# Kernel tuning notes

Hardware: AMD Instinct MI355X
Metric: run time of the kernel (lower is better)

Reference implementation:

```python
import math
import jax, jax.numpy as jnp
import numpy as np

NTYPE, C, H, E = 3, 256, 8, 32  # n_embd=256, n_head=8, edge_dim=32
A1 = 16  # aux_x1 feature dim (aux_x2 dim = E - A1)


def setup_inputs() -> dict:
    key = jax.random.key(0)
    ks = jax.random.split(key, 16)
    B, T1, T2 = 8, 128, 256
    s = 0.02
    return {
        "x1": jax.random.normal(ks[0], (B, T1, C), jnp.float32),
        "x2": jax.random.normal(ks[1], (B, T2, C), jnp.float32),
        "aux_x1": jax.random.normal(ks[2], (B, T1, A1), jnp.float32),
        "aux_x2": jax.random.normal(ks[3], (B, T2, E - A1), jnp.float32),
        "masks": jax.random.randint(ks[4], (NTYPE, B, T1, T2), 0, 2, jnp.int32),
        # per-type linear params, stored (in, out) so y = x @ W + b
        "Wq": jax.random.normal(ks[5], (NTYPE, C, C), jnp.float32) * s,
        "bq": jnp.zeros((NTYPE, C), jnp.float32),
        "Wk": jax.random.normal(ks[6], (NTYPE, C + E, C), jnp.float32) * s,
        "bk": jnp.zeros((NTYPE, C), jnp.float32),
        "Wv": jax.random.normal(ks[7], (NTYPE, C + E, C), jnp.float32) * s,
        "bv": jnp.zeros((NTYPE, C), jnp.float32),
        "Wp": jax.random.normal(ks[8], (NTYPE, C, C), jnp.float32) * s,
        "bp": jnp.zeros((NTYPE, C), jnp.float32),
    }


def _aux_attn(x1, x2, aux_x1, aux_x2, mask, Wq, bq, Wk, bk, Wv, bv, Wp, bp):
    """One AuxCrossAttention type. mask: (B,T1,T2) int."""
    B, T1, _ = x1.shape
    T2 = x2.shape[1]
    hd = C // H
    scale = 1.0 / math.sqrt(hd)

    q = x1 @ Wq + bq  # (B,T1,C)
    # k/v over aug_x2 = [x2 | aux_x1 | aux_x2]; split the linear instead of
    # materializing the (B,T1,T2,C+E) concat (same math by linearity).
    Wk_x, Wk_a1, Wk_a2 = Wk[:C], Wk[C:C + A1], Wk[C + A1:]
    Wv_x, Wv_a1, Wv_a2 = Wv[:C], Wv[C:C + A1], Wv[C + A1:]
    k = (x2 @ Wk_x + aux_x2 @ Wk_a2 + bk)[:, None] + (aux_x1 @ Wk_a1)[:, :, None]  # (B,T1,T2,C)
    v = (x2 @ Wv_x + aux_x2 @ Wv_a2 + bv)[:, None] + (aux_x1 @ Wv_a1)[:, :, None]  # (B,T1,T2,C)

    qh = q.reshape(B, T1, H, hd)
    kh = k.reshape(B, T1, T2, H, hd)
    vh = v.reshape(B, T1, T2, H, hd)

    att = jnp.einsum("bthd,btshd->bhts", qh, kh) * scale  # (B,H,T1,T2)
    valid = (mask != 0)[:, None]  # (B,1,T1,T2)
    att = jnp.where(valid, att, -jnp.inf)
    all_masked = (mask == 0).all(-1)  # (B,T1)
    att = jnp.where(all_masked[:, None, :, None], 0.0, att)
    f = jnp.finfo(att.dtype)
    att = jnp.nan_to_num(att, nan=0.0, posinf=f.max, neginf=f.min)
    att = jax.nn.softmax(att, axis=-1)

    y = jnp.einsum("bhts,btshd->bthd", att, vh).reshape(B, T1, C)
    return y @ Wp + bp


def reference(x1, x2, aux_x1, aux_x2, masks, Wq, bq, Wk, bk, Wv, bv, Wp, bp):
    resid = jnp.zeros_like(x1)
    for i in range(NTYPE):
        resid = resid + _aux_attn(x1, x2, aux_x1, aux_x2, masks[i],
                                  Wq[i], bq[i], Wk[i], bk[i], Wv[i], bv[i], Wp[i], bp[i])
    return resid
```

## Files before the change

kernel.cpp:

```cpp
#include <hip/hip_runtime.h>
#include <hip/hip_bf16.h>

#define NC 256
#define HD 32

typedef __attribute__((ext_vector_type(8))) short short8;
typedef __attribute__((ext_vector_type(4))) short short4v;
typedef __attribute__((ext_vector_type(4))) float f32x4;

__device__ __forceinline__ unsigned short f2bf(float f) {
    union { float f; unsigned u; } v; v.f = f;
    unsigned r = v.u + 0x7fffu + ((v.u >> 16) & 1u);
    return (unsigned short)(r >> 16);
}
__device__ __forceinline__ short8 cvt8(float4 a, float4 b) {
    short8 s;
    s[0] = (short)f2bf(a.x); s[1] = (short)f2bf(a.y);
    s[2] = (short)f2bf(a.z); s[3] = (short)f2bf(a.w);
    s[4] = (short)f2bf(b.x); s[5] = (short)f2bf(b.y);
    s[6] = (short)f2bf(b.z); s[7] = (short)f2bf(b.w);
    return s;
}

__global__ __launch_bounds__(256) void prep_a(
    const float* __restrict__ x1, const float* __restrict__ x2,
    const float* __restrict__ ax1, const float* __restrict__ ax2,
    const int* __restrict__ masks,
    short* __restrict__ x1b, short* __restrict__ A2, short* __restrict__ ax1p,
    unsigned int* __restrict__ mb)
{
    const int bx = blockIdx.x, tid = threadIdx.x;
    const short8 zero8 = {0, 0, 0, 0, 0, 0, 0, 0};

    if (bx < 64) {
        const size_t base = ((size_t)bx * 256 + tid) * 16;
        const float* p = x1 + base;
        float4 a = *(const float4*)p,       b = *(const float4*)(p + 4);
        float4 c = *(const float4*)(p + 8), d = *(const float4*)(p + 12);
        *(short8*)&x1b[base]     = cvt8(a, b);
        *(short8*)&x1b[base + 8] = cvt8(c, d);
    } else if (bx < 352) {
        const int g = (bx - 64) * 256 + tid;
        const int row = g / 36, c8 = g - row * 36;
        short8 s;
        if (c8 < 32) {
            const float* p = x2 + (size_t)row * 256 + c8 * 8;
            s = cvt8(*(const float4*)p, *(const float4*)(p + 4));
        } else if (c8 < 34) {
            const float* p = ax2 + (size_t)row * 16 + (c8 - 32) * 8;
            s = cvt8(*(const float4*)p, *(const float4*)(p + 4));
        } else {
            s = zero8;
        }
        *(short8*)&A2[(size_t)row * 288 + c8 * 8] = s;
    } else if (bx < 356) {
        const int row = (bx - 352) * 256 + tid;
        const float* p = ax1 + (size_t)row * 16;
        float4 a = *(const float4*)p,       b = *(const float4*)(p + 4);
        float4 c = *(const float4*)(p + 8), d = *(const float4*)(p + 12);
        short* o = ax1p + (size_t)row * 32;
        *(short8*)o        = cvt8(a, b);
        *(short8*)(o + 8)  = cvt8(c, d);
        *(short8*)(o + 16) = zero8;
        *(short8*)(o + 24) = zero8;
    } else {
        const int r0 = (bx - 356) * 16;
        const int wave = tid >> 6, lane = tid & 63;
        for (int rr = 0; rr < 16; ++rr) {
            const int row = r0 + rr;
            const int mk = masks[(size_t)row * 256 + tid];
            unsigned long long bal = __ballot(mk != 0);
            if (lane == 0) {
                mb[row * 8 + wave * 2 + 0] = (unsigned int)bal;
                mb[row * 8 + wave * 2 + 1] = (unsigned int)(bal >> 32);
            }
        }
    }
}

__global__ __launch_bounds__(256) void prep_w(
    const float* __restrict__ Wq, const float* __restrict__ Wk,
    const float* __restrict__ Wv, const float* __restrict__ Wp,
    short* __restrict__ WqT, short* __restrict__ WkT, short* __restrict__ WvT,
    short* __restrict__ WvA1T, short* __restrict__ WpT)
{
    const int bx = blockIdx.x, n = threadIdx.x;

    if (bx < 96) {
        const int i = bx >> 5, k8 = bx & 31;
        const float* W = Wq + (size_t)i * 256 * 256;
        short8 s;
#pragma unroll
        for (int j = 0; j < 8; ++j) s[j] = (short)f2bf(W[(size_t)(k8 * 8 + j) * 256 + n]);
        *(short8*)&WqT[(size_t)i * 256 * 256 + (size_t)n * 256 + k8 * 8] = s;
    } else if (bx < 312) {
        const int idx0 = bx - 96;
        const int kv = idx0 / 108, idx = idx0 % 108;
        const int i = idx / 36, k8 = idx % 36;
        const float* W = (kv ? Wv : Wk) + (size_t)i * 288 * 256;
        short* O = (kv ? WvT : WkT) + (size_t)i * 256 * 288;
        short8 s;
#pragma unroll
        for (int j = 0; j < 8; ++j) {
            const int kp = k8 * 8 + j;
            const int src = (kp < 256) ? kp : (kp < 272 ? kp + 16 : -1);
            s[j] = (src >= 0) ? (short)f2bf(W[(size_t)src * 256 + n]) : (short)0;
        }
        *(short8*)&O[(size_t)n * 288 + k8 * 8] = s;
    } else if (bx < 408) {
        const int idx = bx - 312, i = idx >> 5, k8 = idx & 31;
        const float* W = Wp + (size_t)i * 256 * 256;
        short8 s;
#pragma unroll
        for (int j = 0; j < 8; ++j) s[j] = (short)f2bf(W[(size_t)(k8 * 8 + j) * 256 + n]);
        *(short8*)&WpT[(size_t)i * 256 * 256 + (size_t)n * 256 + k8 * 8] = s;
    } else {
        const int i = bx - 408;
        const float* W = Wv + (size_t)i * 288 * 256;
        short* O = WvA1T + (size_t)i * 256 * 32 + (size_t)n * 32;
#pragma unroll
        for (int k8 = 0; k8 < 4; ++k8) {
            short8 s;
#pragma unroll
            for (int j = 0; j < 8; ++j) {
                const int kp = k8 * 8 + j;
                s[j] = (kp < 16) ? (short)f2bf(W[(size_t)(256 + kp) * 256 + n]) : (short)0;
            }
            *(short8*)&O[k8 * 8] = s;
        }
    }
}

__global__ __launch_bounds__(256) void fused_gemm(
    const short* __restrict__ x1b, const short* __restrict__ A2,
    const short* __restrict__ ax1p,
    const short* __restrict__ WqT, const short* __restrict__ WkT,
    const short* __restrict__ WvT, const short* __restrict__ WvA1T,
    const float* __restrict__ bq, const float* __restrict__ bk,
    const float* __restrict__ bv,
    short* __restrict__ qb, short* __restrict__ kbb,
    short* __restrict__ vbT, float* __restrict__ va)
{
    const int bx = blockIdx.x;
    const short *Ab, *Wb;
    const float* bias = nullptr;
    short* outb = nullptr; float* outf = nullptr;
    int LDA, LDW, nsteps, mode, m0, n0;
    if (bx < 48) {
        const int i = bx >> 4, t = bx & 15;
        m0 = (t >> 1) * 128; n0 = (t & 1) * 128;
        Ab = x1b; LDA = 256; Wb = WqT + (size_t)i * 256 * 256; LDW = 256;
        nsteps = 8; bias = bq + i * 256; outb = qb + (size_t)i * 1024 * 256; mode = 0;
    } else if (bx < 144) {
        const int idx = bx - 48, i = idx >> 5, t = idx & 31;
        m0 = (t >> 1) * 128; n0 = (t & 1) * 128;
        Ab = A2; LDA = 288; Wb = WkT + (size_t)i * 256 * 288; LDW = 288;
        nsteps = 9; bias = bk + i * 256; outb = kbb + (size_t)i * 2048 * 256; mode = 0;
    } else if (bx < 240) {
        const int idx = bx - 144, i = idx >> 5, t = idx & 31;
        m0 = (t >> 1) * 128; n0 = (t & 1) * 128;
        Ab = A2; LDA = 288; Wb = WvT + (size_t)i * 256 * 288; LDW = 288;
        nsteps = 9; bias = bv + i * 256; outb = vbT + (size_t)i * 256 * 2048; mode = 1;
    } else {
        const int idx = bx - 240, i = idx >> 4, t = idx & 15;
        m0 = (t >> 1) * 128; n0 = (t & 1) * 128;
        Ab = ax1p; LDA = 32; Wb = WvA1T + (size_t)i * 256 * 32; LDW = 32;
        nsteps = 1; outf = va + (size_t)i * 1024 * 256; mode = 2;
    }

    const int tid = threadIdx.x;
    const int wave = tid >> 6, lane = tid & 63;
    const int wy = wave >> 1, wx = wave & 1;
    const int qd = lane >> 4, ml = lane & 15;

    f32x4 acc[4][4];
#pragma unroll
    for (int a = 0; a < 4; ++a)
#pragma unroll
        for (int b = 0; b < 4; ++b) acc[a][b] = {0.f, 0.f, 0.f, 0.f};

    for (int step = 0; step < nsteps; ++step) {
        short8 af[4], bf[4];
#pragma unroll
        for (int mt = 0; mt < 4; ++mt)
            af[mt] = *(const short8*)&Ab[(size_t)(m0 + wy * 64 + mt * 16 + ml) * LDA + step * 32 + qd * 8];
#pragma unroll
        for (int nt = 0; nt < 4; ++nt)
            bf[nt] = *(const short8*)&Wb[(size_t)(n0 + wx * 64 + nt * 16 + ml) * LDW + step * 32 + qd * 8];
#pragma unroll
        for (int mt = 0; mt < 4; ++mt)
#pragma unroll
            for (int nt = 0; nt < 4; ++nt)
                acc[mt][nt] = __builtin_amdgcn_mfma_f32_16x16x32_bf16(
                    af[mt], bf[nt], acc[mt][nt], 0, 0, 0);
    }

#pragma unroll
    for (int nt = 0; nt < 4; ++nt) {
        const int col = n0 + wx * 64 + nt * 16 + ml;
        const float bsv = bias ? bias[col] : 0.f;
#pragma unroll
        for (int mt = 0; mt < 4; ++mt) {
            const int row0 = m0 + wy * 64 + mt * 16 + qd * 4;
            if (mode == 0) {
#pragma unroll
                for (int r = 0; r < 4; ++r)
                    outb[(size_t)(row0 + r) * 256 + col] = (short)f2bf(acc[mt][nt][r] + bsv);
            } else if (mode == 1) {
                short4v s;
                s.x = (short)f2bf(acc[mt][nt][0] + bsv);
                s.y = (short)f2bf(acc[mt][nt][1] + bsv);
                s.z = (short)f2bf(acc[mt][nt][2] + bsv);
                s.w = (short)f2bf(acc[mt][nt][3] + bsv);
                *(short4v*)&outb[(size_t)col * 2048 + row0] = s;
            } else {
#pragma unroll
                for (int r = 0; r < 4; ++r)
                    outf[(size_t)(row0 + r) * 256 + col] = acc[mt][nt][r];
            }
        }
    }
}

__global__ __launch_bounds__(256) void attn_mfma(
    const short* __restrict__ qb, const short* __restrict__ kbb,
    const short* __restrict__ vbT, const float* __restrict__ va,
    const unsigned int* __restrict__ mb, short* __restrict__ yb)
{
    const int bx = blockIdx.x;
    const int tc = bx & 1, h = (bx >> 1) & 7, b = (bx >> 4) & 7, i = bx >> 7;
    const size_t bb = (size_t)i * 8 + b;

    __shared__ short Ps[4][32 * 16 * 8];

    const int tid = threadIdx.x;
    const int wave = tid >> 6, lane = tid & 63;
    const int ml = lane & 15, qd = lane >> 4;

    const float qscale = 0.17677669529663687f * 1.4426950408889634f;
    short8 af;
    {
        const int t = tc * 64 + wave * 16 + ml;
        short8 qr = *(const short8*)&qb[(bb * 128 + t) * 256 + h * HD + qd * 8];
#pragma unroll
        for (int j = 0; j < 8; ++j) {
            union { float f; unsigned u; } v;
            v.u = ((unsigned)(unsigned short)qr[j]) << 16;
            af[j] = (short)f2bf(v.f * qscale);
        }
    }

    f32x4 sacc[16];
#pragma unroll
    for (int nt = 0; nt < 16; ++nt) sacc[nt] = {0.f, 0.f, 0.f, 0.f};
#pragma unroll
    for (int nt = 0; nt < 16; ++nt) {
        short8 bf = *(const short8*)&kbb[(bb * 256 + nt * 16 + ml) * 256 + h * HD + qd * 8];
        sacc[nt] = __builtin_amdgcn_mfma_f32_16x16x32_bf16(af, bf, sacc[nt], 0, 0, 0);
    }

    const int tb = tc * 64 + wave * 16 + qd * 4;
    uint4 wlo[4], whi[4];
#pragma unroll
    for (int r = 0; r < 4; ++r) {
        const unsigned int* p = mb + (bb * 128 + tb + r) * 8;
        wlo[r] = *(const uint4*)p;
        whi[r] = *(const uint4*)(p + 4);
    }

    f32x4 rs = {0.f, 0.f, 0.f, 0.f};
#pragma unroll
    for (int nt = 0; nt < 16; ++nt) {
#pragma unroll
        for (int r = 0; r < 4; ++r) {
            unsigned int w;
            switch (nt >> 1) {
                case 0: w = wlo[r].x; break; case 1: w = wlo[r].y; break;
                case 2: w = wlo[r].z; break; case 3: w = wlo[r].w; break;
                case 4: w = whi[r].x; break; case 5: w = whi[r].y; break;
                case 6: w = whi[r].z; break; default: w = whi[r].w; break;
            }
            const bool mk = (w >> ((nt & 1) * 16 + ml)) & 1u;
            float e = mk ? __builtin_amdgcn_exp2f(sacc[nt][r]) : 0.f;
            sacc[nt][r] = e;
            rs[r] += e;
        }
    }
#pragma unroll
    for (int off = 1; off <= 8; off <<= 1) {
#pragma unroll
        for (int r = 0; r < 4; ++r) rs[r] += __shfl_xor(rs[r], off);
    }
    f32x4 pinv, pfill;
#pragma unroll
    for (int r = 0; r < 4; ++r) {
        const bool z = (rs[r] == 0.f);
        pinv[r]  = z ? 0.f : 1.f / rs[r];
        pfill[r] = z ? (1.f / 256.f) : 0.f;
    }

    short* Pw = &Ps[wave][0];
#pragma unroll
    for (int nt = 0; nt < 16; ++nt) {
        const int sgrp = 2 * nt + (ml >> 3);
        const int pos = ml & 7;
#pragma unroll
        for (int r = 0; r < 4; ++r) {
            const float p = sacc[nt][r] * pinv[r] + pfill[r];
            Pw[(sgrp * 16 + qd * 4 + r) * 8 + pos] = (short)f2bf(p);
        }
    }

    f32x4 oacc[2];
    oacc[0] = {0.f, 0.f, 0.f, 0.f};
    oacc[1] = {0.f, 0.f, 0.f, 0.f};
    const short* Vb = vbT + (size_t)i * 256 * 2048 + (size_t)b * 256;
#pragma unroll
    for (int ks = 0; ks < 8; ++ks) {
        short8 pa = *(const short8*)&Pw[((ks * 4 + qd) * 16 + ml) * 8];
#pragma unroll
        for (int n2 = 0; n2 < 2; ++n2) {
            short8 vf = *(const short8*)&Vb[(size_t)(h * HD + n2 * 16 + ml) * 2048 + ks * 32 + qd * 8];
            oacc[n2] = __builtin_amdgcn_mfma_f32_16x16x32_bf16(pa, vf, oacc[n2], 0, 0, 0);
        }
    }

#pragma unroll
    for (int n2 = 0; n2 < 2; ++n2) {
        const int d = h * HD + n2 * 16 + ml;
#pragma unroll
        for (int r = 0; r < 4; ++r) {
            const size_t idx = (bb * 128 + tb + r) * 256 + d;
            yb[idx] = (short)f2bf(oacc[n2][r] + va[idx]);
        }
    }
}

__global__ __launch_bounds__(256) void proj2(
    const short* __restrict__ yb, const short* __restrict__ WpT,
    const float* __restrict__ bp, float* __restrict__ out)
{
    const int bx = blockIdx.x;
    const int m0 = (bx >> 2) * 64, n0 = (bx & 3) * 64;
    const int tid = threadIdx.x;
    const int wave = tid >> 6, lane = tid & 63;
    const int wy = wave >> 1, wx = wave & 1;
    const int qd = lane >> 4, ml = lane & 15;

    f32x4 acc[2][2];
#pragma unroll
    for (int a = 0; a < 2; ++a)
#pragma unroll
        for (int b = 0; b < 2; ++b) acc[a][b] = {0.f, 0.f, 0.f, 0.f};

    for (int i = 0; i < 3; ++i) {
        const short* A = yb + (size_t)i * 1024 * 256;
        const short* W = WpT + (size_t)i * 256 * 256;
#pragma unroll
        for (int step = 0; step < 8; ++step) {
            short8 af[2], bf[2];
#pragma unroll
            for (int mt = 0; mt < 2; ++mt)
                af[mt] = *(const short8*)&A[(size_t)(m0 + wy * 32 + mt * 16 + ml) * 256 + step * 32 + qd * 8];
#pragma unroll
            for (int nt = 0; nt < 2; ++nt)
                bf[nt] = *(const short8*)&W[(size_t)(n0 + wx * 32 + nt * 16 + ml) * 256 + step * 32 + qd * 8];
#pragma unroll
            for (int mt = 0; mt < 2; ++mt)
#pragma unroll
                for (int nt = 0; nt < 2; ++nt)
                    acc[mt][nt] = __builtin_amdgcn_mfma_f32_16x16x32_bf16(
                        af[mt], bf[nt], acc[mt][nt], 0, 0, 0);
        }
    }
#pragma unroll
    for (int nt = 0; nt < 2; ++nt) {
        const int col = n0 + wx * 32 + nt * 16 + ml;
        const float b3 = bp[col] + bp[256 + col] + bp[512 + col];
#pragma unroll
        for (int mt = 0; mt < 2; ++mt) {
            const int row0 = m0 + wy * 32 + mt * 16 + qd * 4;
#pragma unroll
            for (int r = 0; r < 4; ++r)
                out[(size_t)(row0 + r) * 256 + col] = acc[mt][nt][r] + b3;
        }
    }
}

extern "C" void kernel_launch(void* const* d_in, const int* in_sizes, int n_in,
                              void* d_out, int out_size, void* d_ws, size_t ws_size,
                              hipStream_t stream)
{
    const float* x1  = (const float*)d_in[0];
    const float* x2  = (const float*)d_in[1];
    const float* ax1 = (const float*)d_in[2];
    const float* ax2 = (const float*)d_in[3];
    const int*   mk  = (const int*)d_in[4];
    const float* Wq  = (const float*)d_in[5];
    const float* bq  = (const float*)d_in[6];
    const float* Wk  = (const float*)d_in[7];
    const float* bk  = (const float*)d_in[8];
    const float* Wv  = (const float*)d_in[9];
    const float* bv  = (const float*)d_in[10];
    const float* Wp  = (const float*)d_in[11];
    const float* bp  = (const float*)d_in[12];

    char* w = (char*)d_ws;
    short* x1b   = (short*)(w + 0);
    short* A2    = (short*)(w + 524288);
    short* ax1p  = (short*)(w + 1703936);
    short* WqT   = (short*)(w + 1769472);
    short* WkT   = (short*)(w + 2162688);
    short* WvT   = (short*)(w + 2605056);
    short* WvA1T = (short*)(w + 3047424);
    short* WpT   = (short*)(w + 3096576);
    unsigned int* mbits = (unsigned int*)(w + 3489792);
    short* qb    = (short*)(w + 3588096);
    short* kbb   = (short*)(w + 5160960);
    short* vbT   = (short*)(w + 8306688);
    float* va    = (float*)(w + 11452416);
    short* yb    = (short*)(w + 14598144);

    prep_a<<<dim3(548), 256, 0, stream>>>(x1, x2, ax1, ax2, mk,
                                          x1b, A2, ax1p, mbits);
    prep_w<<<dim3(411), 256, 0, stream>>>(Wq, Wk, Wv, Wp,
                                          WqT, WkT, WvT, WvA1T, WpT);
    fused_gemm<<<dim3(288), 256, 0, stream>>>(x1b, A2, ax1p, WqT, WkT, WvT,
                                              WvA1T, bq, bk, bv, qb, kbb, vbT, va);
    attn_mfma<<<dim3(384), 256, 0, stream>>>(qb, kbb, vbT, va, mbits, yb);
    proj2<<<dim3(64), 256, 0, stream>>>(yb, WpT, bp, (float*)d_out);
}
```

Before: 130.8 us.

## Fold aux_x1 value term into output projection and merge prep kernels

The aux_x1 contribution to V is the same for every key, and softmax weights sum to one, so that term is moved past attention. A precomputed combined weight (Wv_a1 @ Wp, summed over types) is applied as one extra MFMA step in the final projection. This removes the fp32 va tensor, its GEMM and its per-element read in the attention epilogue. The two prep kernels are merged into one launch, and the q scale is applied in the Q GEMM epilogue instead of in attention. The trade-off is one more bf16 rounding of the folded weight, and the identity needs the softmax rows to sum to one, which still holds for fully masked rows (uniform weights).

```diff
diff --git a/kernel.cpp b/kernel.cpp
--- a/kernel.cpp
+++ b/kernel.cpp
@@ -7,6 +7,8 @@
 typedef __attribute__((ext_vector_type(8))) short short8;
 typedef __attribute__((ext_vector_type(4))) short short4v;
 typedef __attribute__((ext_vector_type(4))) float f32x4;
+
+#define QSC (0.17677669529663687f * 1.4426950408889634f)
 
 __device__ __forceinline__ unsigned short f2bf(float f) {
     union { float f; unsigned u; } v; v.f = f;
@@ -22,12 +24,16 @@
     return s;
 }
 
-__global__ __launch_bounds__(256) void prep_a(
+__global__ __launch_bounds__(256) void prep(
     const float* __restrict__ x1, const float* __restrict__ x2,
     const float* __restrict__ ax1, const float* __restrict__ ax2,
     const int* __restrict__ masks,
+    const float* __restrict__ Wq, const float* __restrict__ Wk,
+    const float* __restrict__ Wv, const float* __restrict__ Wp,
     short* __restrict__ x1b, short* __restrict__ A2, short* __restrict__ ax1p,
-    unsigned int* __restrict__ mb)
+    unsigned int* __restrict__ mb,
+    short* __restrict__ WqT, short* __restrict__ WkT, short* __restrict__ WvT,
+    short* __restrict__ WpT)
 {
     const int bx = blockIdx.x, tid = threadIdx.x;
     const short8 zero8 = {0, 0, 0, 0, 0, 0, 0, 0};
@@ -63,7 +69,7 @@
         *(short8*)(o + 8)  = cvt8(c, d);
         *(short8*)(o + 16) = zero8;
         *(short8*)(o + 24) = zero8;
-    } else {
+    } else if (bx < 548) {
         const int r0 = (bx - 356) * 16;
         const int wave = tid >> 6, lane = tid & 63;
         for (int rr = 0; rr < 16; ++rr) {
@@ -75,28 +81,19 @@
                 mb[row * 8 + wave * 2 + 1] = (unsigned int)(bal >> 32);
             }
         }
-    }
-}
-
-__global__ __launch_bounds__(256) void prep_w(
-    const float* __restrict__ Wq, const float* __restrict__ Wk,
-    const float* __restrict__ Wv, const float* __restrict__ Wp,
-    short* __restrict__ WqT, short* __restrict__ WkT, short* __restrict__ WvT,
-    short* __restrict__ WvA1T, short* __restrict__ WpT)
-{
-    const int bx = blockIdx.x, n = threadIdx.x;
-
-    if (bx < 96) {
-        const int i = bx >> 5, k8 = bx & 31;
+    } else if (bx < 644) {
+        const int idx = bx - 548, i = idx >> 5, k8 = idx & 31;
+        const int n = tid;
         const float* W = Wq + (size_t)i * 256 * 256;
         short8 s;
 #pragma unroll
         for (int j = 0; j < 8; ++j) s[j] = (short)f2bf(W[(size_t)(k8 * 8 + j) * 256 + n]);
         *(short8*)&WqT[(size_t)i * 256 * 256 + (size_t)n * 256 + k8 * 8] = s;
-    } else if (bx < 312) {
-        const int idx0 = bx - 96;
+    } else if (bx < 860) {
+        const int idx0 = bx - 644;
         const int kv = idx0 / 108, idx = idx0 % 108;
         const int i = idx / 36, k8 = idx % 36;
+        const int n = tid;
         const float* W = (kv ? Wv : Wk) + (size_t)i * 288 * 256;
         short* O = (kv ? WvT : WkT) + (size_t)i * 256 * 288;
         short8 s;
@@ -107,71 +104,84 @@
             s[j] = (src >= 0) ? (short)f2bf(W[(size_t)src * 256 + n]) : (short)0;
         }
         *(short8*)&O[(size_t)n * 288 + k8 * 8] = s;
-    } else if (bx < 408) {
-        const int idx = bx - 312, i = idx >> 5, k8 = idx & 31;
+    } else {
+        const int idx = bx - 860, i = idx >> 5, k8 = idx & 31;
+        const int n = tid;
         const float* W = Wp + (size_t)i * 256 * 256;
         short8 s;
 #pragma unroll
         for (int j = 0; j < 8; ++j) s[j] = (short)f2bf(W[(size_t)(k8 * 8 + j) * 256 + n]);
         *(short8*)&WpT[(size_t)i * 256 * 256 + (size_t)n * 256 + k8 * 8] = s;
-    } else {
-        const int i = bx - 408;
-        const float* W = Wv + (size_t)i * 288 * 256;
-        short* O = WvA1T + (size_t)i * 256 * 32 + (size_t)n * 32;
-#pragma unroll
-        for (int k8 = 0; k8 < 4; ++k8) {
-            short8 s;
-#pragma unroll
-            for (int j = 0; j < 8; ++j) {
-                const int kp = k8 * 8 + j;
-                s[j] = (kp < 16) ? (short)f2bf(W[(size_t)(256 + kp) * 256 + n]) : (short)0;
-            }
-            *(short8*)&O[k8 * 8] = s;
-        }
     }
 }
 
 __global__ __launch_bounds__(256) void fused_gemm(
     const short* __restrict__ x1b, const short* __restrict__ A2,
-    const short* __restrict__ ax1p,
     const short* __restrict__ WqT, const short* __restrict__ WkT,
-    const short* __restrict__ WvT, const short* __restrict__ WvA1T,
+    const short* __restrict__ WvT, const float* __restrict__ Wv,
+    const short* __restrict__ WpT,
     const float* __restrict__ bq, const float* __restrict__ bk,
     const float* __restrict__ bv,
     short* __restrict__ qb, short* __restrict__ kbb,
-    short* __restrict__ vbT, float* __restrict__ va)
+    short* __restrict__ vbT, short* __restrict__ WeffT)
 {
     const int bx = blockIdx.x;
+    const int tid = threadIdx.x;
+    const int wave = tid >> 6, lane = tid & 63;
+    const int qd = lane >> 4, ml = lane & 15;
+
+    if (bx == 240) {
+        f32x4 wacc[4];
+#pragma unroll
+        for (int nt = 0; nt < 4; ++nt) wacc[nt] = {0.f, 0.f, 0.f, 0.f};
+        for (int i = 0; i < 3; ++i) {
+            const float* Wvp = Wv + (size_t)i * 288 * 256;
+            const short* Wpt = WpT + (size_t)i * 256 * 256;
+            for (int step = 0; step < 8; ++step) {
+                const float* ap = Wvp + (size_t)(256 + ml) * 256 + step * 32 + qd * 8;
+                short8 af = cvt8(*(const float4*)ap, *(const float4*)(ap + 4));
+#pragma unroll
+                for (int nt = 0; nt < 4; ++nt) {
+                    const int n = (wave * 4 + nt) * 16 + ml;
+                    short8 bf = *(const short8*)&Wpt[(size_t)n * 256 + step * 32 + qd * 8];
+                    wacc[nt] = __builtin_amdgcn_mfma_f32_16x16x32_bf16(af, bf, wacc[nt], 0, 0, 0);
+                }
+            }
+        }
+#pragma unroll
+        for (int nt = 0; nt < 4; ++nt) {
+            const int n = (wave * 4 + nt) * 16 + ml;
+#pragma unroll
+            for (int r = 0; r < 4; ++r) {
+                WeffT[n * 32 + qd * 4 + r] = (short)f2bf(wacc[nt][r]);
+                WeffT[n * 32 + 16 + qd * 4 + r] = 0;
+            }
+        }
+        return;
+    }
+
     const short *Ab, *Wb;
-    const float* bias = nullptr;
-    short* outb = nullptr; float* outf = nullptr;
+    const float* bias;
+    short* outb;
     int LDA, LDW, nsteps, mode, m0, n0;
     if (bx < 48) {
         const int i = bx >> 4, t = bx & 15;
         m0 = (t >> 1) * 128; n0 = (t & 1) * 128;
         Ab = x1b; LDA = 256; Wb = WqT + (size_t)i * 256 * 256; LDW = 256;
-        nsteps = 8; bias = bq + i * 256; outb = qb + (size_t)i * 1024 * 256; mode = 0;
+        nsteps = 8; bias = bq + i * 256; outb = qb + (size_t)i * 1024 * 256; mode = 3;
     } else if (bx < 144) {
         const int idx = bx - 48, i = idx >> 5, t = idx & 31;
         m0 = (t >> 1) * 128; n0 = (t & 1) * 128;
         Ab = A2; LDA = 288; Wb = WkT + (size_t)i * 256 * 288; LDW = 288;
         nsteps = 9; bias = bk + i * 256; outb = kbb + (size_t)i * 2048 * 256; mode = 0;
-    } else if (bx < 240) {
+    } else {
         const int idx = bx - 144, i = idx >> 5, t = idx & 31;
         m0 = (t >> 1) * 128; n0 = (t & 1) * 128;
         Ab = A2; LDA = 288; Wb = WvT + (size_t)i * 256 * 288; LDW = 288;
         nsteps = 9; bias = bv + i * 256; outb = vbT + (size_t)i * 256 * 2048; mode = 1;
-    } else {
-        const int idx = bx - 240, i = idx >> 4, t = idx & 15;
-        m0 = (t >> 1) * 128; n0 = (t & 1) * 128;
-        Ab = ax1p; LDA = 32; Wb = WvA1T + (size_t)i * 256 * 32; LDW = 32;
-        nsteps = 1; outf = va + (size_t)i * 1024 * 256; mode = 2;
-    }
-
-    const int tid = threadIdx.x;
-    const int wave = tid >> 6, lane = tid & 63;
+    }
+
     const int wy = wave >> 1, wx = wave & 1;
-    const int qd = lane >> 4, ml = lane & 15;
 
     f32x4 acc[4][4];
 #pragma unroll
@@ -198,7 +208,7 @@
 #pragma unroll
     for (int nt = 0; nt < 4; ++nt) {
         const int col = n0 + wx * 64 + nt * 16 + ml;
-        const float bsv = bias ? bias[col] : 0.f;
+        const float bsv = bias[col];
 #pragma unroll
         for (int mt = 0; mt < 4; ++mt) {
             const int row0 = m0 + wy * 64 + mt * 16 + qd * 4;
@@ -206,17 +216,17 @@
 #pragma unroll
                 for (int r = 0; r < 4; ++r)
                     outb[(size_t)(row0 + r) * 256 + col] = (short)f2bf(acc[mt][nt][r] + bsv);
-            } else if (mode == 1) {
+            } else if (mode == 3) {
+#pragma unroll
+                for (int r = 0; r < 4; ++r)
+                    outb[(size_t)(row0 + r) * 256 + col] = (short)f2bf((acc[mt][nt][r] + bsv) * QSC);
+            } else {
                 short4v s;
                 s.x = (short)f2bf(acc[mt][nt][0] + bsv);
                 s.y = (short)f2bf(acc[mt][nt][1] + bsv);
                 s.z = (short)f2bf(acc[mt][nt][2] + bsv);
                 s.w = (short)f2bf(acc[mt][nt][3] + bsv);
                 *(short4v*)&outb[(size_t)col * 2048 + row0] = s;
-            } else {
-#pragma unroll
-                for (int r = 0; r < 4; ++r)
-                    outf[(size_t)(row0 + r) * 256 + col] = acc[mt][nt][r];
             }
         }
     }
@@ -224,8 +234,8 @@
 
 __global__ __launch_bounds__(256) void attn_mfma(
     const short* __restrict__ qb, const short* __restrict__ kbb,
-    const short* __restrict__ vbT, const float* __restrict__ va,
-    const unsigned int* __restrict__ mb, short* __restrict__ yb)
+    const short* __restrict__ vbT, const unsigned int* __restrict__ mb,
+    short* __restrict__ yb)
 {
     const int bx = blockIdx.x;
     const int tc = bx & 1, h = (bx >> 1) & 7, b = (bx >> 4) & 7, i = bx >> 7;
@@ -237,18 +247,8 @@
     const int wave = tid >> 6, lane = tid & 63;
     const int ml = lane & 15, qd = lane >> 4;
 
-    const float qscale = 0.17677669529663687f * 1.4426950408889634f;
-    short8 af;
-    {
-        const int t = tc * 64 + wave * 16 + ml;
-        short8 qr = *(const short8*)&qb[(bb * 128 + t) * 256 + h * HD + qd * 8];
-#pragma unroll
-        for (int j = 0; j < 8; ++j) {
-            union { float f; unsigned u; } v;
-            v.u = ((unsigned)(unsigned short)qr[j]) << 16;
-            af[j] = (short)f2bf(v.f * qscale);
-        }
-    }
+    const int t = tc * 64 + wave * 16 + ml;
+    short8 af = *(const short8*)&qb[(bb * 128 + t) * 256 + h * HD + qd * 8];
 
     f32x4 sacc[16];
 #pragma unroll
@@ -331,13 +331,14 @@
 #pragma unroll
         for (int r = 0; r < 4; ++r) {
             const size_t idx = (bb * 128 + tb + r) * 256 + d;
-            yb[idx] = (short)f2bf(oacc[n2][r] + va[idx]);
+            yb[idx] = (short)f2bf(oacc[n2][r]);
         }
     }
 }
 
 __global__ __launch_bounds__(256) void proj2(
     const short* __restrict__ yb, const short* __restrict__ WpT,
+    const short* __restrict__ ax1p, const short* __restrict__ WeffT,
     const float* __restrict__ bp, float* __restrict__ out)
 {
     const int bx = blockIdx.x;
@@ -372,6 +373,21 @@
                     acc[mt][nt] = __builtin_amdgcn_mfma_f32_16x16x32_bf16(
                         af[mt], bf[nt], acc[mt][nt], 0, 0, 0);
         }
+    }
+    {
+        short8 af[2], bf[2];
+#pragma unroll
+        for (int mt = 0; mt < 2; ++mt)
+            af[mt] = *(const short8*)&ax1p[(size_t)(m0 + wy * 32 + mt * 16 + ml) * 32 + qd * 8];
+#pragma unroll
+        for (int nt = 0; nt < 2; ++nt)
+            bf[nt] = *(const short8*)&WeffT[(size_t)(n0 + wx * 32 + nt * 16 + ml) * 32 + qd * 8];
+#pragma unroll
+        for (int mt = 0; mt < 2; ++mt)
+#pragma unroll
+            for (int nt = 0; nt < 2; ++nt)
+                acc[mt][nt] = __builtin_amdgcn_mfma_f32_16x16x32_bf16(
+                    af[mt], bf[nt], acc[mt][nt], 0, 0, 0);
     }
 #pragma unroll
     for (int nt = 0; nt < 2; ++nt) {
@@ -412,21 +428,18 @@
     short* WqT   = (short*)(w + 1769472);
     short* WkT   = (short*)(w + 2162688);
     short* WvT   = (short*)(w + 2605056);
-    short* WvA1T = (short*)(w + 3047424);
-    short* WpT   = (short*)(w + 3096576);
-    unsigned int* mbits = (unsigned int*)(w + 3489792);
-    short* qb    = (short*)(w + 3588096);
-    short* kbb   = (short*)(w + 5160960);
-    short* vbT   = (short*)(w + 8306688);
-    float* va    = (float*)(w + 11452416);
-    short* yb    = (short*)(w + 14598144);
-
-    prep_a<<<dim3(548), 256, 0, stream>>>(x1, x2, ax1, ax2, mk,
-                                          x1b, A2, ax1p, mbits);
-    prep_w<<<dim3(411), 256, 0, stream>>>(Wq, Wk, Wv, Wp,
-                                          WqT, WkT, WvT, WvA1T, WpT);
-    fused_gemm<<<dim3(288), 256, 0, stream>>>(x1b, A2, ax1p, WqT, WkT, WvT,
-                                              WvA1T, bq, bk, bv, qb, kbb, vbT, va);
-    attn_mfma<<<dim3(384), 256, 0, stream>>>(qb, kbb, vbT, va, mbits, yb);
-    proj2<<<dim3(64), 256, 0, stream>>>(yb, WpT, bp, (float*)d_out);
-}
+    short* WpT   = (short*)(w + 3047424);
+    unsigned int* mbits = (unsigned int*)(w + 3440640);
+    short* WeffT = (short*)(w + 3538944);
+    short* qb    = (short*)(w + 3555328);
+    short* kbb   = (short*)(w + 5128192);
+    short* vbT   = (short*)(w + 8273920);
+    short* yb    = (short*)(w + 11419648);
+
+    prep<<<dim3(956), 256, 0, stream>>>(x1, x2, ax1, ax2, mk, Wq, Wk, Wv, Wp,
+                                        x1b, A2, ax1p, mbits, WqT, WkT, WvT, WpT);
+    fused_gemm<<<dim3(241), 256, 0, stream>>>(x1b, A2, WqT, WkT, WvT, Wv, WpT,
+                                              bq, bk, bv, qb, kbb, vbT, WeffT);
+    attn_mfma<<<dim3(384), 256, 0, stream>>>(qb, kbb, vbT, mbits, yb);
+    proj2<<<dim3(64), 256, 0, stream>>>(yb, WpT, ax1p, WeffT, bp, (float*)d_out);
+}
```

Result: no change. 133.3 us (+1.9%).
